# Optimization experiments

Hardware: AMD Instinct MI355X
Metric: run time of the kernel (lower is better)

The kernel has to match this reference:

```python
import jax, jax.numpy as jnp
import numpy as np

# ---- instant-NGP / torch-ngp style 2D hash-grid constants (from __init__ config) ----
NUM_LEVELS = 16
LEVEL_DIM = 2
BASE_RES = 16
MAX_PARAMS = 2 ** 19  # log2_hashmap_size = 19
PER_LEVEL_SCALE = float(np.exp2(np.log2(2048.0 / 16.0) / (NUM_LEVELS - 1)))  # desired_resolution overrides per_level_scale
PRIME_Y = np.uint32(2654435761)
DIVIDE_FACTOR = 1.0
FEAT_DIM = NUM_LEVELS * LEVEL_DIM  # 32
MAX_LEVELS = 12  # set_level_auto(500000)

def _meta():
    scales, sizes, offsets = [], [], [0]
    for l in range(NUM_LEVELS):
        scale = BASE_RES * PER_LEVEL_SCALE ** l - 1.0
        res = int(np.ceil(scale)) + 1
        params = min(MAX_PARAMS, res * res)
        params = int(np.ceil(params / 8) * 8)  # align to 8 like torch-ngp
        scales.append(scale)
        sizes.append((res, params))
        offsets.append(offsets[-1] + params)
    return scales, sizes, offsets

SCALES, SIZES, OFFSETS = _meta()
TOTAL_PARAMS = OFFSETS[-1]  # 2761312


def hash_grid_encode(x, table):
    """x: [N,2] in [0,1]; table: [TOTAL_PARAMS, LEVEL_DIM]. Returns [N, FEAT_DIM]."""
    feats = []
    for l in range(NUM_LEVELS):  # fixed small unroll over levels
        scale = SCALES[l]
        res, size = SIZES[l]
        off = OFFSETS[l]
        pos = x * scale + 0.5
        g0 = jnp.floor(pos)
        frac = pos - g0
        g0 = g0.astype(jnp.uint32)
        out = jnp.zeros((x.shape[0], LEVEL_DIM), x.dtype)
        for cx in (0, 1):  # bilinear corners
            wx = frac[:, 0] if cx else 1.0 - frac[:, 0]
            gx = g0[:, 0] + np.uint32(cx)
            for cy in (0, 1):
                wy = frac[:, 1] if cy else 1.0 - frac[:, 1]
                gy = g0[:, 1] + np.uint32(cy)
                if res * res <= size:  # dense (tiled) indexing at coarse levels
                    idx = (gx + gy * np.uint32(res)) % np.uint32(size)
                else:  # spatial hash at fine levels
                    idx = (gx ^ (gy * PRIME_Y)) % np.uint32(size)
                out = out + (wx * wy)[:, None] * table[off + idx.astype(jnp.int32)]
        feats.append(out)
    return jnp.concatenate(feats, axis=-1)


def setup_inputs() -> dict:
    key = jax.random.key(0)
    k1, k2, k3, k4 = jax.random.split(key, 4)
    N = 2_000_000
    init = lambda k: (jax.random.uniform(k, (TOTAL_PARAMS, LEVEL_DIM), jnp.float32) * 2.0 - 1.0) * 1e-4
    return {
        "input": jax.random.uniform(k1, (N, 3), jnp.float32),  # points in [0,1)
        "table_xy": init(k2),
        "table_yz": init(k3),
        "table_xz": init(k4),
        "step": 20000,
    }


def reference(input, table_xy, table_yz, table_xz, step):
    level = min(step // 1000 + 1, MAX_LEVELS)  # static python int -> static mask
    mask = (jnp.arange(FEAT_DIM) < 2 * level).astype(input.dtype)[None, :]
    x = input / DIVIDE_FACTOR
    xy = hash_grid_encode(x[:, (0, 1)], table_xy) * mask
    yz = hash_grid_encode(x[:, (1, 2)], table_yz) * mask
    xz = hash_grid_encode(x[:, (0, 2)], table_xz) * mask
    return xy + yz + xz
```

## Files before the change

### kernel.cpp

```cpp
#include <hip/hip_runtime.h>
#include <cmath>
#include <cstdint>

namespace {

constexpr int kLevels = 12;
constexpr int kFeat = 32;
constexpr int kBatch = 6;
constexpr unsigned kNB = 32768;

typedef float f32x4 __attribute__((ext_vector_type(4)));
typedef float f32x4u __attribute__((ext_vector_type(4), aligned(8)));

struct LevelMeta {
  float scale;
  unsigned res;
  unsigned size;
  unsigned off;
};

struct Meta {
  LevelMeta lv[kLevels];
};

__device__ inline unsigned spread5(unsigned v) {
  v &= 31u;
  v = (v | (v << 8)) & 0x0000100Fu;
  v = (v | (v << 4)) & 0x000010C3u;
  v = (v | (v << 2)) & 0x00001249u;
  return v;
}

__device__ inline unsigned bucket_of(float x, float y, float z) {
  unsigned xi = (unsigned)fminf(fmaxf(x * 32.0f, 0.0f), 31.0f);
  unsigned yi = (unsigned)fminf(fmaxf(y * 32.0f, 0.0f), 31.0f);
  unsigned zi = (unsigned)fminf(fmaxf(z * 32.0f, 0.0f), 31.0f);
  return spread5(xi) | (spread5(yi) << 1) | (spread5(zi) << 2);
}

template <typename AccFn>
__device__ inline void gather_planes(float px, float py, float pz,
                                     const float* __restrict__ txy,
                                     const float* __restrict__ tyz,
                                     const float* __restrict__ txz,
                                     const Meta& meta, float* acc) {
  auto do_plane = [&](float c0, float c1, const float* __restrict__ tabf) {
    const float2* __restrict__ tab = reinterpret_cast<const float2*>(tabf);
#pragma unroll
    for (int h = 0; h < kLevels / kBatch; ++h) {
      f32x4 r0[kBatch], r1[kBatch];
      float fxs[kBatch], fys[kBatch];
      unsigned wrap0 = 0, wrap1 = 0;

#pragma unroll
      for (int j = 0; j < kBatch; ++j) {
        const int l = h * kBatch + j;
        const float s = meta.lv[l].scale;
        const unsigned res = meta.lv[l].res;
        const unsigned size = meta.lv[l].size;
        const float2* tb = tab + meta.lv[l].off;

        const float posx = fmaf(c0, s, 0.5f);
        const float posy = fmaf(c1, s, 0.5f);
        const float g0x = floorf(posx);
        const float g0y = floorf(posy);
        fxs[j] = posx - g0x;
        fys[j] = posy - g0y;
        const unsigned ix = (unsigned)g0x;
        const unsigned iy = (unsigned)g0y;

        unsigned i00 = ix + iy * res;
        unsigned i01 = i00 + res;
        if (i01 >= size) i01 -= size;
        wrap0 |= (i00 == size - 1u) ? (1u << j) : 0u;
        wrap1 |= (i01 == size - 1u) ? (1u << j) : 0u;
        r0[j] = *reinterpret_cast<const f32x4u*>(tb + i00);
        r1[j] = *reinterpret_cast<const f32x4u*>(tb + i01);
      }

#pragma unroll
      for (int j = 0; j < kBatch; ++j) {
        const int l = h * kBatch + j;
        const float2* tb = tab + meta.lv[l].off;
        const float2 tf = *tb;

        const float fx = fxs[j];
        const float fy = fys[j];
        const bool w0 = (wrap0 >> j) & 1u;
        const bool w1 = (wrap1 >> j) & 1u;
        const float t10x = w0 ? tf.x : r0[j].z;
        const float t10y = w0 ? tf.y : r0[j].w;
        const float t11x = w1 ? tf.x : r1[j].z;
        const float t11y = w1 ? tf.y : r1[j].w;

        const float w00 = (1.0f - fx) * (1.0f - fy);
        const float w01 = (1.0f - fx) * fy;
        const float w10 = fx * (1.0f - fy);
        const float w11 = fx * fy;

        acc[2 * l + 0] += w00 * r0[j].x + w01 * r1[j].x + w10 * t10x + w11 * t11x;
        acc[2 * l + 1] += w00 * r0[j].y + w01 * r1[j].y + w10 * t10y + w11 * t11y;
      }
    }
  };
  do_plane(px, py, txy);
  do_plane(py, pz, tyz);
  do_plane(px, pz, txz);
}

}


__global__ __launch_bounds__(256) void k_hist(const float* __restrict__ xyz,
                                              unsigned* __restrict__ counts, int n) {
  const int i = blockIdx.x * blockDim.x + threadIdx.x;
  if (i >= n) return;
  atomicAdd(&counts[bucket_of(xyz[3 * i], xyz[3 * i + 1], xyz[3 * i + 2])], 1u);
}

__global__ __launch_bounds__(1024) void k_scan(const unsigned* __restrict__ counts,
                                               unsigned* __restrict__ cursor) {
  __shared__ unsigned part[1024];
  const int t = threadIdx.x;
  const int base = t * 32;
  unsigned loc[32];
  unsigned run = 0;
#pragma unroll
  for (int j = 0; j < 32; ++j) { loc[j] = run; run += counts[base + j]; }
  part[t] = run;
  __syncthreads();
  for (int off = 1; off < 1024; off <<= 1) {
    unsigned v = (t >= off) ? part[t - off] : 0u;
    __syncthreads();
    part[t] += v;
    __syncthreads();
  }
  const unsigned ebase = part[t] - run;
#pragma unroll
  for (int j = 0; j < 32; ++j) cursor[base + j] = ebase + loc[j];
}

__global__ __launch_bounds__(256) void k_scatter(const float* __restrict__ xyz,
                                                 unsigned* __restrict__ cursor,
                                                 f32x4* __restrict__ sorted, int n) {
  const int i = blockIdx.x * blockDim.x + threadIdx.x;
  if (i >= n) return;
  const float x = xyz[3 * i], y = xyz[3 * i + 1], z = xyz[3 * i + 2];
  const unsigned pos = atomicAdd(&cursor[bucket_of(x, y, z)], 1u);
  f32x4 v;
  v.x = x; v.y = y; v.z = z; v.w = __uint_as_float((unsigned)i);
  sorted[pos] = v;
}


__global__ __launch_bounds__(256) void k_main_sorted(
    const f32x4* __restrict__ sorted,
    const float* __restrict__ txy,
    const float* __restrict__ tyz,
    const float* __restrict__ txz,
    const int* __restrict__ step_ptr,
    float* __restrict__ out,
    int n, Meta meta)
{
  __shared__ float lds[4 * 8 * 260];
  __shared__ unsigned idxs[256];

  const int tid = threadIdx.x;
  const int wid = tid >> 6;
  const int lane = tid & 63;
  const int g = blockIdx.x * 256 + tid;
  const bool valid = g < n;
  const f32x4 s = sorted[valid ? g : (n - 1)];
  const unsigned row = valid ? __float_as_uint(s.w) : 0xFFFFFFFFu;

  const int step = *step_ptr;
  int level = step / 1000 + 1;
  level = level > kLevels ? kLevels : level;
  const int active = 2 * level;

  float acc[2 * kLevels];
#pragma unroll
  for (int k = 0; k < 2 * kLevels; ++k) acc[k] = 0.0f;

  gather_planes<int>(s.x, s.y, s.z, txy, tyz, txz, meta, acc);

#pragma unroll
  for (int k = 0; k < 2 * kLevels; ++k)
    if (k >= active) acc[k] = 0.0f;

  float* wlds = lds + wid * (8 * 260);
#pragma unroll
  for (int c = 0; c < 8; ++c) {
    f32x4 v;
    v.x = c < 6 ? acc[4 * c + 0] : 0.0f;
    v.y = c < 6 ? acc[4 * c + 1] : 0.0f;
    v.z = c < 6 ? acc[4 * c + 2] : 0.0f;
    v.w = c < 6 ? acc[4 * c + 3] : 0.0f;
    *reinterpret_cast<f32x4*>(wlds + c * 260 + lane * 4) = v;
  }
  idxs[tid] = row;
  __syncthreads();

#pragma unroll
  for (int q = 0; q < 8; ++q) {
    const int p = q * 8 + (lane >> 3);
    const int c = lane & 7;
    const unsigned r = idxs[wid * 64 + p];
    const f32x4 v = *reinterpret_cast<const f32x4*>(wlds + c * 260 + p * 4);
    if (r != 0xFFFFFFFFu)
      __builtin_nontemporal_store(v, reinterpret_cast<f32x4*>(out) + (size_t)r * 8 + c);
  }
}


__global__ __launch_bounds__(256) void k_fused_linear(
    const float* __restrict__ xyz,
    const float* __restrict__ txy,
    const float* __restrict__ tyz,
    const float* __restrict__ txz,
    const int* __restrict__ step_ptr,
    float* __restrict__ out,
    int n, Meta meta)
{
  __shared__ float lds[4 * 2048];
  const int tid = threadIdx.x;
  const int wid = tid >> 6;
  const int lane = tid & 63;
  const int bbase = blockIdx.x * 256;
  const int i = bbase + tid;
  const int pi = i < n ? i : (n - 1);

  const int step = *step_ptr;
  int level = step / 1000 + 1;
  level = level > kLevels ? kLevels : level;
  const int active = 2 * level;

  float acc[2 * kLevels];
#pragma unroll
  for (int k = 0; k < 2 * kLevels; ++k) acc[k] = 0.0f;

  gather_planes<int>(xyz[3 * pi], xyz[3 * pi + 1], xyz[3 * pi + 2],
                     txy, tyz, txz, meta, acc);

#pragma unroll
  for (int k = 0; k < 2 * kLevels; ++k)
    if (k >= active) acc[k] = 0.0f;

  float* wlds = lds + wid * 2048;
#pragma unroll
  for (int c = 0; c < 8; ++c) {
    f32x4 v;
    v.x = c < 6 ? acc[4 * c + 0] : 0.0f;
    v.y = c < 6 ? acc[4 * c + 1] : 0.0f;
    v.z = c < 6 ? acc[4 * c + 2] : 0.0f;
    v.w = c < 6 ? acc[4 * c + 3] : 0.0f;
    *reinterpret_cast<f32x4*>(wlds + c * 256 + lane * 4) = v;
  }
  __syncthreads();

  const long long wbase = (long long)bbase + wid * 64;
  f32x4* obase = reinterpret_cast<f32x4*>(out) + wbase * 8;
#pragma unroll
  for (int q = 0; q < 8; ++q) {
    const int p = q * 8 + (lane >> 3);
    const int c = lane & 7;
    const f32x4 v = *reinterpret_cast<const f32x4*>(wlds + c * 256 + p * 4);
    if (wbase + p < n)
      __builtin_nontemporal_store(v, obase + q * 64 + lane);
  }
}

extern "C" void kernel_launch(void* const* d_in, const int* in_sizes, int n_in,
                              void* d_out, int out_size, void* d_ws, size_t ws_size,
                              hipStream_t stream) {
  const float* xyz = (const float*)d_in[0];
  const float* txy = (const float*)d_in[1];
  const float* tyz = (const float*)d_in[2];
  const float* txz = (const float*)d_in[3];
  const int* step  = (const int*)d_in[4];
  float* out = (float*)d_out;
  const int n = in_sizes[0] / 3;

  Meta meta;
  unsigned off = 0;
  const double pls = std::exp2(std::log2(2048.0 / 16.0) / 15.0);
  for (int l = 0; l < 16; ++l) {
    const double scale = 16.0 * std::pow(pls, (double)l) - 1.0;
    const unsigned res = (unsigned)std::ceil(scale) + 1u;
    unsigned long long params = (unsigned long long)res * (unsigned long long)res;
    if (params > (1ull << 19)) params = (1ull << 19);
    params = ((params + 7ull) / 8ull) * 8ull;
    if (l < kLevels) {
      meta.lv[l].scale = (float)scale;
      meta.lv[l].res = res;
      meta.lv[l].size = (unsigned)params;
      meta.lv[l].off = off;
    }
    off += (unsigned)params;
  }

  const dim3 block(256);
  const dim3 grid((unsigned)((n + 255) / 256));

  const size_t sorted_off = 256 * 1024;
  const size_t need = sorted_off + (size_t)n * sizeof(f32x4);

  if (ws_size >= need) {
    unsigned* counts = (unsigned*)d_ws;
    unsigned* cursor = counts + kNB;
    f32x4* sorted = (f32x4*)((char*)d_ws + sorted_off);

    hipMemsetAsync(counts, 0, kNB * sizeof(unsigned), stream);
    hipLaunchKernelGGL(k_hist, grid, block, 0, stream, xyz, counts, n);
    hipLaunchKernelGGL(k_scan, dim3(1), dim3(1024), 0, stream, counts, cursor);
    hipLaunchKernelGGL(k_scatter, grid, block, 0, stream, xyz, cursor, sorted, n);
    hipLaunchKernelGGL(k_main_sorted, grid, block, 0, stream,
                       sorted, txy, tyz, txz, step, out, n, meta);
  } else {
    hipLaunchKernelGGL(k_fused_linear, grid, block, 0, stream,
                       xyz, txy, tyz, txz, step, out, n, meta);
  }
}
```

Baseline: 556.1 us.

## Stage per-wave bounding-box table tiles in LDS for sorted-point gathers

```diff
diff --git a/kernel.cpp b/kernel.cpp
--- a/kernel.cpp
+++ b/kernel.cpp
@@ -5,23 +5,14 @@
 namespace {
 
 constexpr int kLevels = 12;
-constexpr int kFeat = 32;
-constexpr int kBatch = 6;
 constexpr unsigned kNB = 32768;
+constexpr unsigned kTileCap = 512;
 
 typedef float f32x4 __attribute__((ext_vector_type(4)));
 typedef float f32x4u __attribute__((ext_vector_type(4), aligned(8)));
 
-struct LevelMeta {
-  float scale;
-  unsigned res;
-  unsigned size;
-  unsigned off;
-};
-
-struct Meta {
-  LevelMeta lv[kLevels];
-};
+struct LevelMeta { float scale; unsigned res; unsigned size; unsigned off; };
+struct Meta { LevelMeta lv[kLevels]; };
 
 __device__ inline unsigned spread5(unsigned v) {
   v &= 31u;
@@ -36,76 +27,6 @@
   unsigned yi = (unsigned)fminf(fmaxf(y * 32.0f, 0.0f), 31.0f);
   unsigned zi = (unsigned)fminf(fmaxf(z * 32.0f, 0.0f), 31.0f);
   return spread5(xi) | (spread5(yi) << 1) | (spread5(zi) << 2);
-}
-
-template <typename AccFn>
-__device__ inline void gather_planes(float px, float py, float pz,
-                                     const float* __restrict__ txy,
-                                     const float* __restrict__ tyz,
-                                     const float* __restrict__ txz,
-                                     const Meta& meta, float* acc) {
-  auto do_plane = [&](float c0, float c1, const float* __restrict__ tabf) {
-    const float2* __restrict__ tab = reinterpret_cast<const float2*>(tabf);
-#pragma unroll
-    for (int h = 0; h < kLevels / kBatch; ++h) {
-      f32x4 r0[kBatch], r1[kBatch];
-      float fxs[kBatch], fys[kBatch];
-      unsigned wrap0 = 0, wrap1 = 0;
-
-#pragma unroll
-      for (int j = 0; j < kBatch; ++j) {
-        const int l = h * kBatch + j;
-        const float s = meta.lv[l].scale;
-        const unsigned res = meta.lv[l].res;
-        const unsigned size = meta.lv[l].size;
-        const float2* tb = tab + meta.lv[l].off;
-
-        const float posx = fmaf(c0, s, 0.5f);
-        const float posy = fmaf(c1, s, 0.5f);
-        const float g0x = floorf(posx);
-        const float g0y = floorf(posy);
-        fxs[j] = posx - g0x;
-        fys[j] = posy - g0y;
-        const unsigned ix = (unsigned)g0x;
-        const unsigned iy = (unsigned)g0y;
-
-        unsigned i00 = ix + iy * res;
-        unsigned i01 = i00 + res;
-        if (i01 >= size) i01 -= size;
-        wrap0 |= (i00 == size - 1u) ? (1u << j) : 0u;
-        wrap1 |= (i01 == size - 1u) ? (1u << j) : 0u;
-        r0[j] = *reinterpret_cast<const f32x4u*>(tb + i00);
-        r1[j] = *reinterpret_cast<const f32x4u*>(tb + i01);
-      }
-
-#pragma unroll
-      for (int j = 0; j < kBatch; ++j) {
-        const int l = h * kBatch + j;
-        const float2* tb = tab + meta.lv[l].off;
-        const float2 tf = *tb;
-
-        const float fx = fxs[j];
-        const float fy = fys[j];
-        const bool w0 = (wrap0 >> j) & 1u;
-        const bool w1 = (wrap1 >> j) & 1u;
-        const float t10x = w0 ? tf.x : r0[j].z;
-        const float t10y = w0 ? tf.y : r0[j].w;
-        const float t11x = w1 ? tf.x : r1[j].z;
-        const float t11y = w1 ? tf.y : r1[j].w;
-
-        const float w00 = (1.0f - fx) * (1.0f - fy);
-        const float w01 = (1.0f - fx) * fy;
-        const float w10 = fx * (1.0f - fy);
-        const float w11 = fx * fy;
-
-        acc[2 * l + 0] += w00 * r0[j].x + w01 * r1[j].x + w10 * t10x + w11 * t11x;
-        acc[2 * l + 1] += w00 * r0[j].y + w01 * r1[j].y + w10 * t10y + w11 * t11y;
-      }
-    }
-  };
-  do_plane(px, py, txy);
-  do_plane(py, pz, tyz);
-  do_plane(px, pz, txz);
 }
 
 }
@@ -162,7 +83,8 @@
     float* __restrict__ out,
     int n, Meta meta)
 {
-  __shared__ float lds[4 * 8 * 260];
+  __shared__ float stg[4 * 2080];
+  __shared__ float2 tiles[4 * kTileCap];
   __shared__ unsigned idxs[256];
 
   const int tid = threadIdx.x;
@@ -176,28 +98,115 @@
   const int step = *step_ptr;
   int level = step / 1000 + 1;
   level = level > kLevels ? kLevels : level;
-  const int active = 2 * level;
-
-  float acc[2 * kLevels];
-#pragma unroll
-  for (int k = 0; k < 2 * kLevels; ++k) acc[k] = 0.0f;
-
-  gather_planes<int>(s.x, s.y, s.z, txy, tyz, txz, meta, acc);
-
-#pragma unroll
-  for (int k = 0; k < 2 * kLevels; ++k)
-    if (k >= active) acc[k] = 0.0f;
-
-  float* wlds = lds + wid * (8 * 260);
-#pragma unroll
-  for (int c = 0; c < 8; ++c) {
-    f32x4 v;
-    v.x = c < 6 ? acc[4 * c + 0] : 0.0f;
-    v.y = c < 6 ? acc[4 * c + 1] : 0.0f;
-    v.z = c < 6 ? acc[4 * c + 2] : 0.0f;
-    v.w = c < 6 ? acc[4 * c + 3] : 0.0f;
-    *reinterpret_cast<f32x4*>(wlds + c * 260 + lane * 4) = v;
-  }
+
+  float mnx = s.x, mxx = s.x, mny = s.y, mxy = s.y, mnz = s.z, mxz = s.z;
+#pragma unroll
+  for (int m = 1; m < 64; m <<= 1) {
+    mnx = fminf(mnx, __shfl_xor(mnx, m)); mxx = fmaxf(mxx, __shfl_xor(mxx, m));
+    mny = fminf(mny, __shfl_xor(mny, m)); mxy = fmaxf(mxy, __shfl_xor(mxy, m));
+    mnz = fminf(mnz, __shfl_xor(mnz, m)); mxz = fmaxf(mxz, __shfl_xor(mxz, m));
+  }
+
+  float2* tile = &tiles[wid * kTileCap];
+  float* wlds = stg + wid * 2080;
+
+  {
+    const f32x4 z = {0.0f, 0.0f, 0.0f, 0.0f};
+    *reinterpret_cast<f32x4*>(wlds + 6 * 260 + lane * 4) = z;
+    *reinterpret_cast<f32x4*>(wlds + 7 * 260 + lane * 4) = z;
+  }
+
+  for (int l = 0; l < kLevels; ++l) {
+    const LevelMeta lm = meta.lv[l];
+    float a0 = 0.0f, a1 = 0.0f;
+
+    auto plane = [&](float c0, float c1, float lo0, float hi0, float lo1, float hi1,
+                     const float* __restrict__ tabf) {
+      const float2* __restrict__ tab = reinterpret_cast<const float2*>(tabf) + lm.off;
+
+      const float posx = fmaf(c0, lm.scale, 0.5f);
+      const float posy = fmaf(c1, lm.scale, 0.5f);
+      const float g0x = floorf(posx);
+      const float g0y = floorf(posy);
+      const float fx = posx - g0x;
+      const float fy = posy - g0y;
+      const unsigned ix = (unsigned)g0x;
+      const unsigned iy = (unsigned)g0y;
+
+      const unsigned ix0 = (unsigned)floorf(fmaf(lo0, lm.scale, 0.5f));
+      const unsigned ix1 = (unsigned)floorf(fmaf(hi0, lm.scale, 0.5f));
+      const unsigned iy0 = (unsigned)floorf(fmaf(lo1, lm.scale, 0.5f));
+      const unsigned iy1 = (unsigned)floorf(fmaf(hi1, lm.scale, 0.5f));
+      const unsigned C = ix1 - ix0 + 2u;
+      const unsigned R = iy1 - iy0 + 2u;
+      const unsigned S = C | 1u;
+
+      float2 q00, q01, q10, q11;
+      if (C <= 64u && R * S <= kTileCap) {
+        const unsigned kk = 32u - __builtin_clz(C - 1u);
+        const unsigned rpi = 64u >> kk;
+        const unsigned I = (R + rpi - 1u) >> (6u - kk);
+        const unsigned rr = lane >> kk;
+        const unsigned cc = lane & ((1u << kk) - 1u);
+
+        float2 v0 = make_float2(0.0f, 0.0f);
+        unsigned d0 = rr * S + cc;
+        bool ok0 = (cc < C) & (rr < R);
+        {
+          unsigned gi = (iy0 + rr) * lm.res + ix0 + cc;
+          if (gi >= lm.size) gi -= lm.size;
+          if (ok0) v0 = tab[gi];
+        }
+        for (unsigned t = 1; t < I; ++t) {
+          const unsigned r = t * rpi + rr;
+          float2 v1 = make_float2(0.0f, 0.0f);
+          const bool ok1 = (cc < C) & (r < R);
+          unsigned gi = (iy0 + r) * lm.res + ix0 + cc;
+          if (gi >= lm.size) gi -= lm.size;
+          if (ok1) v1 = tab[gi];
+          if (ok0) tile[d0] = v0;
+          v0 = v1; d0 = r * S + cc; ok0 = ok1;
+        }
+        if (ok0) tile[d0] = v0;
+
+        const unsigned a = (iy - iy0) * S + (ix - ix0);
+        q00 = tile[a];
+        q10 = tile[a + 1];
+        q01 = tile[a + S];
+        q11 = tile[a + S + 1];
+      } else {
+        unsigned i00 = ix + iy * lm.res;
+        unsigned i01 = i00 + lm.res;
+        if (i01 >= lm.size) i01 -= lm.size;
+        const f32x4 r0 = *reinterpret_cast<const f32x4u*>(tab + i00);
+        const f32x4 r1 = *reinterpret_cast<const f32x4u*>(tab + i01);
+        const float2 tf = *tab;
+        const bool w0 = (i00 == lm.size - 1u);
+        const bool w1 = (i01 == lm.size - 1u);
+        q00 = make_float2(r0.x, r0.y);
+        q10 = w0 ? tf : make_float2(r0.z, r0.w);
+        q01 = make_float2(r1.x, r1.y);
+        q11 = w1 ? tf : make_float2(r1.z, r1.w);
+      }
+
+      const float w00 = (1.0f - fx) * (1.0f - fy);
+      const float w01 = (1.0f - fx) * fy;
+      const float w10 = fx * (1.0f - fy);
+      const float w11 = fx * fy;
+      a0 += w00 * q00.x + w01 * q01.x + w10 * q10.x + w11 * q11.x;
+      a1 += w00 * q00.y + w01 * q01.y + w10 * q10.y + w11 * q11.y;
+    };
+
+    plane(s.x, s.y, mnx, mxx, mny, mxy, txy);
+    plane(s.y, s.z, mny, mxy, mnz, mxz, tyz);
+    plane(s.x, s.z, mnx, mxx, mnz, mxz, txz);
+
+    float2 pr = (l < level) ? make_float2(a0, a1) : make_float2(0.0f, 0.0f);
+    const int chunk = l >> 1;
+    const int ofs = (l & 1) * 2;
+    *reinterpret_cast<float2*>(wlds + chunk * 260 + lane * 4 + ofs) = pr;
+  }
+
   idxs[tid] = row;
   __syncthreads();
 
@@ -235,12 +244,42 @@
   level = level > kLevels ? kLevels : level;
   const int active = 2 * level;
 
+  const float px = xyz[3 * pi], py = xyz[3 * pi + 1], pz = xyz[3 * pi + 2];
   float acc[2 * kLevels];
 #pragma unroll
   for (int k = 0; k < 2 * kLevels; ++k) acc[k] = 0.0f;
 
-  gather_planes<int>(xyz[3 * pi], xyz[3 * pi + 1], xyz[3 * pi + 2],
-                     txy, tyz, txz, meta, acc);
+  auto do_plane = [&](float c0, float c1, const float* __restrict__ tabf) {
+    const float2* __restrict__ tab = reinterpret_cast<const float2*>(tabf);
+#pragma unroll
+    for (int l = 0; l < kLevels; ++l) {
+      const LevelMeta lm = meta.lv[l];
+      const float2* tb = tab + lm.off;
+      const float posx = fmaf(c0, lm.scale, 0.5f);
+      const float posy = fmaf(c1, lm.scale, 0.5f);
+      const float g0x = floorf(posx), g0y = floorf(posy);
+      const float fx = posx - g0x, fy = posy - g0y;
+      const unsigned ix = (unsigned)g0x, iy = (unsigned)g0y;
+      unsigned i00 = ix + iy * lm.res;
+      unsigned i01 = i00 + lm.res;
+      if (i01 >= lm.size) i01 -= lm.size;
+      const f32x4 r0 = *reinterpret_cast<const f32x4u*>(tb + i00);
+      const f32x4 r1 = *reinterpret_cast<const f32x4u*>(tb + i01);
+      const float2 tf = *tb;
+      const bool w0 = (i00 == lm.size - 1u), w1 = (i01 == lm.size - 1u);
+      const float t10x = w0 ? tf.x : r0.z, t10y = w0 ? tf.y : r0.w;
+      const float t11x = w1 ? tf.x : r1.z, t11y = w1 ? tf.y : r1.w;
+      const float w00 = (1.0f - fx) * (1.0f - fy);
+      const float w01 = (1.0f - fx) * fy;
+      const float w10 = fx * (1.0f - fy);
+      const float w11 = fx * fy;
+      acc[2 * l + 0] += w00 * r0.x + w01 * r1.x + w10 * t10x + w11 * t11x;
+      acc[2 * l + 1] += w00 * r0.y + w01 * r1.y + w10 * t10y + w11 * t11y;
+    }
+  };
+  do_plane(px, py, txy);
+  do_plane(py, pz, tyz);
+  do_plane(px, pz, txz);
 
 #pragma unroll
   for (int k = 0; k < 2 * kLevels; ++k)
```

Result: no change. 559.4 us (+0.6%).
